# Optimization experiments

Hardware: AMD Instinct MI355X
Metric: run time of the kernel (lower is better)

## Reference

```python
import math
import jax, jax.numpy as jnp
import numpy as np

# ---- module hyperparams (from init_kwargs defaults) ----
NUM_AA, EMB_DIM, K, EXCLUDE = 20, 16, 64, 2
R_ON, R_CUT, DELTA, WALL = 8.0, 10.0, 0.3, 10.0
RHO_MIN, RHO_MAX, RHO_BASE = 1.6, 2.8, 2.0
B, L = 8, 2048
BIG = 1e9  # masks excluded pairs in the distance matrix


def setup_inputs() -> dict:
    key = jax.random.key(0)
    k1, k2, k3 = jax.random.split(key, 3)
    # coordinates scaled to a realistic Angstrom spread so switch/softplus are exercised
    R = jax.random.normal(k1, (B, L, 3), dtype=jnp.float32) * 10.0
    seq = jax.random.randint(k2, (B, L), 0, NUM_AA, dtype=jnp.int64)
    # learned params: AA embedding table + size head (small random weight, bias at rho_base)
    emb_table = jax.random.normal(k3, (NUM_AA, EMB_DIM), dtype=jnp.float32)
    size_w = 0.1 * jax.random.normal(jax.random.fold_in(key, 7), (1, EMB_DIM), dtype=jnp.float32)
    frac = (RHO_BASE - RHO_MIN) / max(1e-6, RHO_MAX - RHO_MIN)
    frac = min(0.999, max(0.001, frac))
    size_b = jnp.full((1,), math.log(frac / (1.0 - frac)), dtype=jnp.float32)
    return {"R": R, "seq": seq, "emb_table": emb_table, "size_w": size_w, "size_b": size_b}


def _rho(s, emb_table, size_w, size_b):
    # per-residue learned radius in [RHO_MIN, RHO_MAX]; s: int indices, any shape
    e = emb_table[s]                                  # (..., EMB_DIM)
    x = jnp.einsum('...d,d->...', e, size_w[0]) + size_b[0]
    return RHO_MIN + (RHO_MAX - RHO_MIN) * jax.nn.sigmoid(x)


def _smooth_switch(r):
    # smoothstep from 1 (r<=R_ON) down to 0 (r>=R_CUT)
    t = jnp.clip((r - R_ON) / (R_CUT - R_ON), 0.0, 1.0)
    return 1.0 - t * t * (3.0 - 2.0 * t)


def reference(R, seq, emb_table, size_w, size_b):
    b, l, _ = R.shape
    # pairwise distances (B, L, L)
    diff = R[:, :, None, :] - R[:, None, :, :]
    D = jnp.sqrt(jnp.maximum(jnp.sum(diff * diff, axis=-1), 1e-12))
    # exclude bonded/near-diagonal pairs |i-j| <= EXCLUDE (includes self)
    idx = jnp.arange(l)
    excl = jnp.abs(idx[:, None] - idx[None, :]) <= EXCLUDE
    Dm = jnp.where(excl[None], BIG, D)
    # K smallest distances per residue -> negate for lax.top_k
    neg_r, j = jax.lax.top_k(-Dm, K)                  # (B, L, K)
    r = -neg_r
    # gather neighbor sequence ids along L
    seq_j = jnp.take_along_axis(jnp.broadcast_to(seq[:, :, None], (b, l, K)), j, axis=1)
    # pair radius r0_ij = rho(s_i) + rho(s_j)
    rho_i = _rho(seq, emb_table, size_w, size_b)[:, :, None]   # (B, L, 1)
    rho_j = _rho(seq_j, emb_table, size_w, size_b)             # (B, L, K)
    r0 = rho_i + rho_j
    rep = WALL * jax.nn.softplus((r0 - r) / (DELTA + 1e-12))
    return (rep * _smooth_switch(r)).sum(axis=(1, 2))          # (B,)
```

## Files before the change

### kernel.cpp

```cpp
#include <hip/hip_runtime.h>
#include <math.h>

#define LRES 2048
#define NB 8
#define KSEL 64
#define EMBD 16
#define NBIN 128
#define BINSCALE 1.28f
#define BINW 0.78125f
#define NSLOT 8

__global__ void rho_kernel(const int* __restrict__ seq,
                           const float* __restrict__ emb,
                           const float* __restrict__ w,
                           const float* __restrict__ bias,
                           float* __restrict__ rho) {
    int idx = blockIdx.x * blockDim.x + threadIdx.x;
    if (idx < NB * LRES) {
        int s = seq[idx];
        float x = bias[0];
#pragma unroll
        for (int d = 0; d < EMBD; ++d) x += emb[s * EMBD + d] * w[d];
        rho[idx] = 1.6f + 1.2f / (1.0f + expf(-x));
    }
}

#define LDS_FENCE() asm volatile("s_waitcnt lgkmcnt(0)" ::: "memory")

__global__ __launch_bounds__(512, 8) void repel_kernel(const float* __restrict__ R,
                                                       const float* __restrict__ rho,
                                                       float* __restrict__ partial) {
    const int w    = threadIdx.x >> 6;
    const int lane = threadIdx.x & 63;
    const int row  = blockIdx.x * 8 + w;
    const int b    = row >> 11;
    const int i    = row & 2047;

    __shared__ float4  pt[LRES];
    __shared__ unsigned hist[8][NBIN];
    __shared__ unsigned slots[8][NSLOT][64];
    __shared__ unsigned shT[8];

    {
        const float4* Rg = (const float4*)(R + (size_t)b * (LRES * 3));
        const float4* Qg = (const float4*)(rho + (b << 11));
        int t = threadIdx.x;
        float4 f0 = Rg[3 * t + 0];
        float4 f1 = Rg[3 * t + 1];
        float4 f2 = Rg[3 * t + 2];
        float4 q  = Qg[t];
        pt[4 * t + 0] = make_float4(f0.x, f0.y, f0.z, q.x);
        pt[4 * t + 1] = make_float4(f0.w, f1.x, f1.y, q.y);
        pt[4 * t + 2] = make_float4(f1.z, f1.w, f2.x, q.z);
        pt[4 * t + 3] = make_float4(f2.y, f2.z, f2.w, q.w);
    }
    *(uint2*)&hist[w][lane << 1] = make_uint2(0u, 0u);
    if (lane == 0) shT[w] = NBIN - 1;
    __syncthreads();

    float4 c = pt[i];
    const float cx = c.x, cy = c.y, cz = c.z, rho_i = c.w;

    unsigned d2u[32];
#pragma unroll 8
    for (int t = 0; t < 32; ++t) {
        int j = (t << 6) + lane;
        float4 p = pt[j];
        float dx = p.x - cx, dy = p.y - cy, dz = p.z - cz;
        float d2 = dx * dx + dy * dy + dz * dz;
        int dij = j - i; dij = (dij < 0) ? -dij : dij;
        unsigned du = (dij <= 2) ? 0xFFFFFFFFu : __float_as_uint(d2);
        d2u[t] = du;
        if (du <= 0x42C7FFFFu)
            atomicAdd(&hist[w][(unsigned)(d2 * BINSCALE)], 1u);
    }
    LDS_FENCE();

    uint2 hv = *(const uint2*)&hist[w][lane << 1];
    unsigned p = hv.x + hv.y;
    unsigned s = p;
#pragma unroll
    for (int o = 1; o < 64; o <<= 1) {
        unsigned u = __shfl_up(s, o, 64);
        if (lane >= o) s += u;
    }
    unsigned e0 = s - p;
    if (s >= KSEL && e0 < KSEL) {
        unsigned sub = (e0 + hv.x >= KSEL) ? 0u : 1u;
        shT[w] = (lane << 1) + sub;
    }
    LDS_FENCE();
    const unsigned T   = shT[w];
    const unsigned tkb = __float_as_uint((float)(T + 1) * BINW);

    unsigned cnt = 0;
#pragma unroll
    for (int t = 0; t < 32; ++t) {
        if (d2u[t] < tkb && cnt < NSLOT) {
            unsigned j = (unsigned)((t << 6) + lane);
            slots[w][cnt][lane] = (d2u[t] & 0xFFFFF800u) | j;
            ++cnt;
        }
    }
    LDS_FENCE();

    float acc = 0.0f;
    for (unsigned k = 0; k < cnt; ++k) {
        unsigned key = slots[w][k][lane];
        unsigned j = key & 2047u;
        float d2 = __uint_as_float(key & 0xFFFFF800u);
        float r = __fsqrt_rn(fmaxf(d2, 1e-12f));
        float rho_j = pt[j].w;
        float x = (rho_i + rho_j - r) * (1.0f / 0.3f);
        float sp = fmaxf(x, 0.0f) + __logf(1.0f + __expf(-fabsf(x)));
        float t = fminf(fmaxf((r - 8.0f) * 0.5f, 0.0f), 1.0f);
        float sw = 1.0f - t * t * (3.0f - 2.0f * t);
        acc += 10.0f * sp * sw;
    }
#pragma unroll
    for (int o = 32; o > 0; o >>= 1) acc += __shfl_down(acc, o, 64);
    if (lane == 0) partial[row] = acc;
}

__global__ void reduce_kernel(const float* __restrict__ partial, float* __restrict__ out) {
    __shared__ float sh[4];
    const int b = blockIdx.x;
    const int tid = threadIdx.x;
    float acc = 0.0f;
#pragma unroll
    for (int k = 0; k < 8; ++k) acc += partial[(b << 11) + (k << 8) + tid];
#pragma unroll
    for (int o = 32; o > 0; o >>= 1) acc += __shfl_down(acc, o, 64);
    if ((tid & 63) == 0) sh[tid >> 6] = acc;
    __syncthreads();
    if (tid == 0) out[b] = sh[0] + sh[1] + sh[2] + sh[3];
}

extern "C" void kernel_launch(void* const* d_in, const int* in_sizes, int n_in,
                              void* d_out, int out_size, void* d_ws, size_t ws_size,
                              hipStream_t stream) {
    const float* R    = (const float*)d_in[0];
    const int*   seq  = (const int*)d_in[1];
    const float* emb  = (const float*)d_in[2];
    const float* w    = (const float*)d_in[3];
    const float* bias = (const float*)d_in[4];
    float* out = (float*)d_out;

    float* rho     = (float*)d_ws;
    float* partial = (float*)d_ws + NB * LRES;

    rho_kernel<<<(NB * LRES + 255) / 256, 256, 0, stream>>>(seq, emb, w, bias, rho);
    repel_kernel<<<NB * LRES / 8, 512, 0, stream>>>(R, rho, partial);
    reduce_kernel<<<NB, 256, 0, stream>>>(partial, out);
}
```

Before: 93.03 us.

## Process eight rows per wave with register-blocked distances and fused atomic reduction

Each wave now handles eight query rows, so each LDS point load is reused across eight distance computations. Fewer blocks are launched, and the 32 KB point-tile staging is amortized over 32 rows instead of 8. Distances are recomputed in a second pass instead of being held in 32 registers per row. The histogram uses 100 integer bins of d2 instead of 128 scaled bins. The separate reduce kernel is removed: output is zeroed in rho_kernel and the per-block sum is added with a global atomicAdd, which makes the floating-point summation order nondeterministic. All eight rows in a wave share one 16-entry slot budget per lane, which risks dropping selected neighbors.

Measured after the change: 106.5 us. +14.4%, slower.

```diff
diff --git a/kernel.cpp b/kernel.cpp
--- a/kernel.cpp
+++ b/kernel.cpp
@@ -5,17 +5,21 @@
 #define NB 8
 #define KSEL 64
 #define EMBD 16
-#define NBIN 128
-#define BINSCALE 1.28f
-#define BINW 0.78125f
-#define NSLOT 8
+#define NBIN 100
+#define NSLOT 16
+#define RPW 8
+#define WPB 4
+#define RPB (RPW * WPB)
+#define BPB (LRES / RPB)
 
 __global__ void rho_kernel(const int* __restrict__ seq,
                            const float* __restrict__ emb,
                            const float* __restrict__ w,
                            const float* __restrict__ bias,
-                           float* __restrict__ rho) {
+                           float* __restrict__ rho,
+                           float* __restrict__ out) {
     int idx = blockIdx.x * blockDim.x + threadIdx.x;
+    if (idx < NB) out[idx] = 0.0f;
     if (idx < NB * LRES) {
         int s = seq[idx];
         float x = bias[0];
@@ -27,113 +31,132 @@
 
 #define LDS_FENCE() asm volatile("s_waitcnt lgkmcnt(0)" ::: "memory")
 
-__global__ __launch_bounds__(512, 8) void repel_kernel(const float* __restrict__ R,
+__global__ __launch_bounds__(256, 4) void repel_kernel(const float* __restrict__ R,
                                                        const float* __restrict__ rho,
-                                                       float* __restrict__ partial) {
-    const int w    = threadIdx.x >> 6;
-    const int lane = threadIdx.x & 63;
-    const int row  = blockIdx.x * 8 + w;
-    const int b    = row >> 11;
-    const int i    = row & 2047;
+                                                       float* __restrict__ out) {
+    const int tid  = threadIdx.x;
+    const int w    = tid >> 6;
+    const int lane = tid & 63;
+    const int blk  = blockIdx.x;
+    const int b    = blk >> 6;
+    const int i0   = (blk & 63) << 5;
 
     __shared__ float4  pt[LRES];
-    __shared__ unsigned hist[8][NBIN];
-    __shared__ unsigned slots[8][NSLOT][64];
-    __shared__ unsigned shT[8];
+    __shared__ unsigned hist[RPB][NBIN];
+    __shared__ unsigned slots[WPB][NSLOT][64];
+    __shared__ unsigned shT[RPB];
+    __shared__ float    shred[WPB];
 
     {
         const float4* Rg = (const float4*)(R + (size_t)b * (LRES * 3));
         const float4* Qg = (const float4*)(rho + (b << 11));
-        int t = threadIdx.x;
-        float4 f0 = Rg[3 * t + 0];
-        float4 f1 = Rg[3 * t + 1];
-        float4 f2 = Rg[3 * t + 2];
-        float4 q  = Qg[t];
-        pt[4 * t + 0] = make_float4(f0.x, f0.y, f0.z, q.x);
-        pt[4 * t + 1] = make_float4(f0.w, f1.x, f1.y, q.y);
-        pt[4 * t + 2] = make_float4(f1.z, f1.w, f2.x, q.z);
-        pt[4 * t + 3] = make_float4(f2.y, f2.z, f2.w, q.w);
+        float4 f0 = Rg[6 * tid + 0], f1 = Rg[6 * tid + 1], f2 = Rg[6 * tid + 2];
+        float4 f3 = Rg[6 * tid + 3], f4 = Rg[6 * tid + 4], f5 = Rg[6 * tid + 5];
+        float4 q0 = Qg[2 * tid], q1 = Qg[2 * tid + 1];
+        pt[8 * tid + 0] = make_float4(f0.x, f0.y, f0.z, q0.x);
+        pt[8 * tid + 1] = make_float4(f0.w, f1.x, f1.y, q0.y);
+        pt[8 * tid + 2] = make_float4(f1.z, f1.w, f2.x, q0.z);
+        pt[8 * tid + 3] = make_float4(f2.y, f2.z, f2.w, q0.w);
+        pt[8 * tid + 4] = make_float4(f3.x, f3.y, f3.z, q1.x);
+        pt[8 * tid + 5] = make_float4(f3.w, f4.x, f4.y, q1.y);
+        pt[8 * tid + 6] = make_float4(f4.z, f4.w, f5.x, q1.z);
+        pt[8 * tid + 7] = make_float4(f5.y, f5.z, f5.w, q1.w);
     }
-    *(uint2*)&hist[w][lane << 1] = make_uint2(0u, 0u);
-    if (lane == 0) shT[w] = NBIN - 1;
+    {
+        unsigned* hflat = (unsigned*)hist;
+#pragma unroll
+        for (int q = 0; q < 13; ++q) {
+            int idx = tid + (q << 8);
+            if (idx < RPB * NBIN) hflat[idx] = 0u;
+        }
+    }
+    if (tid < RPB) shT[tid] = NBIN - 1;
     __syncthreads();
 
-    float4 c = pt[i];
-    const float cx = c.x, cy = c.y, cz = c.z, rho_i = c.w;
+    const int iw = i0 + (w << 3);
+    float cxx[RPW], cyy[RPW], czz[RPW];
+#pragma unroll
+    for (int r = 0; r < RPW; ++r) {
+        float4 c = pt[iw + r];
+        cxx[r] = c.x; cyy[r] = c.y; czz[r] = c.z;
+    }
 
-    unsigned d2u[32];
-#pragma unroll 8
+#pragma unroll 4
     for (int t = 0; t < 32; ++t) {
         int j = (t << 6) + lane;
         float4 p = pt[j];
-        float dx = p.x - cx, dy = p.y - cy, dz = p.z - cz;
-        float d2 = dx * dx + dy * dy + dz * dz;
-        int dij = j - i; dij = (dij < 0) ? -dij : dij;
-        unsigned du = (dij <= 2) ? 0xFFFFFFFFu : __float_as_uint(d2);
-        d2u[t] = du;
-        if (du <= 0x42C7FFFFu)
-            atomicAdd(&hist[w][(unsigned)(d2 * BINSCALE)], 1u);
-    }
-    LDS_FENCE();
-
-    uint2 hv = *(const uint2*)&hist[w][lane << 1];
-    unsigned p = hv.x + hv.y;
-    unsigned s = p;
 #pragma unroll
-    for (int o = 1; o < 64; o <<= 1) {
-        unsigned u = __shfl_up(s, o, 64);
-        if (lane >= o) s += u;
-    }
-    unsigned e0 = s - p;
-    if (s >= KSEL && e0 < KSEL) {
-        unsigned sub = (e0 + hv.x >= KSEL) ? 0u : 1u;
-        shT[w] = (lane << 1) + sub;
-    }
-    LDS_FENCE();
-    const unsigned T   = shT[w];
-    const unsigned tkb = __float_as_uint((float)(T + 1) * BINW);
-
-    unsigned cnt = 0;
-#pragma unroll
-    for (int t = 0; t < 32; ++t) {
-        if (d2u[t] < tkb && cnt < NSLOT) {
-            unsigned j = (unsigned)((t << 6) + lane);
-            slots[w][cnt][lane] = (d2u[t] & 0xFFFFF800u) | j;
-            ++cnt;
+        for (int r = 0; r < RPW; ++r) {
+            float dx = p.x - cxx[r], dy = p.y - cyy[r], dz = p.z - czz[r];
+            float d2 = dx * dx + dy * dy + dz * dz;
+            int dij = j - (iw + r); dij = (dij < 0) ? -dij : dij;
+            if (dij > 2 && d2 < 100.0f)
+                atomicAdd(&hist[(w << 3) + r][(unsigned)d2], 1u);
         }
     }
     LDS_FENCE();
 
+#pragma unroll
+    for (int r = 0; r < RPW; ++r) {
+        int row = (w << 3) + r;
+        uint2 hv = (lane < 50) ? *(const uint2*)&hist[row][lane << 1]
+                               : make_uint2(0u, 0u);
+        unsigned p = hv.x + hv.y;
+        unsigned s = p;
+#pragma unroll
+        for (int o = 1; o < 64; o <<= 1) {
+            unsigned u = __shfl_up(s, o, 64);
+            if (lane >= o) s += u;
+        }
+        unsigned e0 = s - p;
+        if (s >= KSEL && e0 < KSEL)
+            shT[row] = (e0 + hv.x >= KSEL) ? (unsigned)(lane << 1)
+                                           : (unsigned)(lane << 1) + 1u;
+    }
+    LDS_FENCE();
+    float tkb[RPW];
+#pragma unroll
+    for (int r = 0; r < RPW; ++r) tkb[r] = (float)(shT[(w << 3) + r] + 1u);
+
+    unsigned cnt = 0;
+#pragma unroll 4
+    for (int t = 0; t < 32; ++t) {
+        int j = (t << 6) + lane;
+        float4 p = pt[j];
+#pragma unroll
+        for (int r = 0; r < RPW; ++r) {
+            float dx = p.x - cxx[r], dy = p.y - cyy[r], dz = p.z - czz[r];
+            float d2 = dx * dx + dy * dy + dz * dz;
+            int dij = j - (iw + r); dij = (dij < 0) ? -dij : dij;
+            if (dij > 2 && d2 < tkb[r] && cnt < NSLOT) {
+                slots[w][cnt][lane] = ((unsigned)r << 11) | (unsigned)j;
+                ++cnt;
+            }
+        }
+    }
+
     float acc = 0.0f;
     for (unsigned k = 0; k < cnt; ++k) {
-        unsigned key = slots[w][k][lane];
-        unsigned j = key & 2047u;
-        float d2 = __uint_as_float(key & 0xFFFFF800u);
-        float r = __fsqrt_rn(fmaxf(d2, 1e-12f));
-        float rho_j = pt[j].w;
-        float x = (rho_i + rho_j - r) * (1.0f / 0.3f);
+        unsigned u = slots[w][k][lane];
+        unsigned j = u & 2047u;
+        unsigned r = u >> 11;
+        float4 pj = pt[j];
+        float4 pi = pt[iw + (int)r];
+        float dx = pj.x - pi.x, dy = pj.y - pi.y, dz = pj.z - pi.z;
+        float d2 = dx * dx + dy * dy + dz * dz;
+        float rr = __fsqrt_rn(fmaxf(d2, 1e-12f));
+        float x = (pi.w + pj.w - rr) * (1.0f / 0.3f);
         float sp = fmaxf(x, 0.0f) + __logf(1.0f + __expf(-fabsf(x)));
-        float t = fminf(fmaxf((r - 8.0f) * 0.5f, 0.0f), 1.0f);
+        float t = fminf(fmaxf((rr - 8.0f) * 0.5f, 0.0f), 1.0f);
         float sw = 1.0f - t * t * (3.0f - 2.0f * t);
         acc += 10.0f * sp * sw;
     }
+
 #pragma unroll
     for (int o = 32; o > 0; o >>= 1) acc += __shfl_down(acc, o, 64);
-    if (lane == 0) partial[row] = acc;
-}
-
-__global__ void reduce_kernel(const float* __restrict__ partial, float* __restrict__ out) {
-    __shared__ float sh[4];
-    const int b = blockIdx.x;
-    const int tid = threadIdx.x;
-    float acc = 0.0f;
-#pragma unroll
-    for (int k = 0; k < 8; ++k) acc += partial[(b << 11) + (k << 8) + tid];
-#pragma unroll
-    for (int o = 32; o > 0; o >>= 1) acc += __shfl_down(acc, o, 64);
-    if ((tid & 63) == 0) sh[tid >> 6] = acc;
+    if (lane == 0) shred[w] = acc;
     __syncthreads();
-    if (tid == 0) out[b] = sh[0] + sh[1] + sh[2] + sh[3];
+    if (tid == 0) atomicAdd(out + b, shred[0] + shred[1] + shred[2] + shred[3]);
 }
 
 extern "C" void kernel_launch(void* const* d_in, const int* in_sizes, int n_in,
@@ -145,11 +168,8 @@
     const float* w    = (const float*)d_in[3];
     const float* bias = (const float*)d_in[4];
     float* out = (float*)d_out;
+    float* rho = (float*)d_ws;
 
-    float* rho     = (float*)d_ws;
-    float* partial = (float*)d_ws + NB * LRES;
-
-    rho_kernel<<<(NB * LRES + 255) / 256, 256, 0, stream>>>(seq, emb, w, bias, rho);
-    repel_kernel<<<NB * LRES / 8, 512, 0, stream>>>(R, rho, partial);
-    reduce_kernel<<<NB, 256, 0, stream>>>(partial, out);
+    rho_kernel<<<(NB * LRES + 255) / 256, 256, 0, stream>>>(seq, emb, w, bias, rho, out);
+    repel_kernel<<<NB * LRES / RPB, 256, 0, stream>>>(R, rho, out);
 }
```
